# Optimization experiments

Hardware: AMD Instinct MI355X
Metric: run time of the kernel (lower is better)

The kernel has to match this reference:

```python
import jax, jax.numpy as jnp
import numpy as np

GROUPS = 8
NEG_SLOPE = 0.1
EPS = 1e-5


def group_norm(x, gamma, beta):
    # x: (B, N, C). Matches torch GroupNorm applied on (B, C, N):
    # normalize over (channels-in-group, N) per batch per group.
    B, N, C = x.shape
    xg = x.reshape(B, N, GROUPS, C // GROUPS)
    mean = xg.mean(axis=(1, 3), keepdims=True)
    var = xg.var(axis=(1, 3), keepdims=True)
    xg = (xg - mean) * jax.lax.rsqrt(var + EPS)
    return xg.reshape(B, N, C) * gamma + beta


def unary_block(x, W, b, gamma, beta):
    # Linear -> GroupNorm -> LeakyReLU(0.1)
    h = jnp.einsum('bnc,cd->bnd', x, W) + b
    h = group_norm(h, gamma, beta)
    return jnp.where(h >= 0, h, NEG_SLOPE * h)


def setup_inputs() -> dict:
    key = jax.random.key(0)
    ks = jax.random.split(key, 16)
    B, N, M, K, Cin, Cout = 4, 8192, 32768, 16, 128, 128
    inp = {
        'q_feats': jax.random.normal(ks[0], (B, N, Cin), jnp.float32),
        's_feats': jax.random.normal(ks[1], (B, M, Cin), jnp.float32),
        'q_points': jax.random.normal(ks[2], (B, N, 3), jnp.float32),
        's_points': jax.random.normal(ks[3], (B, N, K, 3), jnp.float32),
        'downsample_indices': jax.random.randint(ks[4], (B, N, K), 0, M, jnp.int32),
    }
    sc1 = 1.0 / np.sqrt(Cin)
    sc2 = 1.0 / np.sqrt(Cout)
    inp['W1'] = jax.random.uniform(ks[5], (Cin, Cout), jnp.float32, -sc1, sc1)
    inp['b1'] = jnp.zeros((Cout,), jnp.float32)
    inp['g1'] = jnp.ones((Cout,), jnp.float32)
    inp['be1'] = jnp.zeros((Cout,), jnp.float32)
    inp['W2'] = jax.random.uniform(ks[6], (Cout, Cout), jnp.float32, -sc2, sc2)
    inp['b2'] = jnp.zeros((Cout,), jnp.float32)
    inp['g2'] = jnp.ones((Cout,), jnp.float32)
    inp['be2'] = jnp.zeros((Cout,), jnp.float32)
    inp['W3'] = jax.random.uniform(ks[7], (Cout, Cout), jnp.float32, -sc2, sc2)
    inp['b3'] = jnp.zeros((Cout,), jnp.float32)
    inp['g3'] = jnp.ones((Cout,), jnp.float32)
    inp['be3'] = jnp.zeros((Cout,), jnp.float32)
    return inp


def reference(q_feats, s_feats, q_points, s_points, downsample_indices,
              W1, b1, g1, be1, W2, b2, g2, be2, W3, b3, g3, be3):
    # knn_gather: (B, N, K, C) gathered from (B, M, C)
    grouped = jax.vmap(lambda f, i: f[i])(s_feats, downsample_indices)
    # inverse-squared-distance weights over K neighbors
    d2 = jnp.sum((s_points - q_points[:, :, None, :]) ** 2, axis=-1)  # (B,N,K)
    w = 1.0 / (d2 + 1e-8)
    w = w / jnp.sum(w, axis=-1, keepdims=True)
    latent = jnp.sum(grouped * w[..., None], axis=2)  # (B,N,C)
    h = unary_block(latent, W1, b1, g1, be1)
    h = unary_block(h, W2, b2, g2, be2)
    return unary_block(h + q_feats, W3, b3, g3, be3)
```

## Files before the change

### kernel.cpp

```cpp
#include <hip/hip_runtime.h>


constexpr int NPB = 8192;
constexpr int BN  = 32768;
constexpr int CH  = 128;
constexpr int KNB = 16;
constexpr int MS  = 32768;
constexpr int NG  = 8;
constexpr int CG  = 16;
constexpr int RPB = 64;
constexpr int NBLK = BN / RPB;
constexpr int BPB  = NPB / RPB;
constexpr int XS = 152;
constexpr int WS = 152;

typedef short short8 __attribute__((ext_vector_type(8)));
typedef float floatx4 __attribute__((ext_vector_type(4)));

static __device__ __forceinline__ unsigned short f2bs(float f) {
    unsigned int u = __builtin_bit_cast(unsigned int, f);
    unsigned int r = (u + 0x7fffu + ((u >> 16) & 1u)) >> 16;
    return (unsigned short)r;
}
static __device__ __forceinline__ float bs2f(unsigned short s) {
    unsigned int u = ((unsigned int)s) << 16;
    return __builtin_bit_cast(float, u);
}

__global__ __launch_bounds__(256) void k_prep(
    const float* __restrict__ W1, const float* __restrict__ W2,
    const float* __restrict__ W3,
    unsigned short* __restrict__ Wt1, unsigned short* __restrict__ Wf2,
    unsigned short* __restrict__ Wf3)
{
    const int bi = blockIdx.x;
    const int w  = bi >> 6;
    const int i  = bi & 63;
    const int el = i * 256 + threadIdx.x;
    const int n  = el >> 7, k = el & 127;
    const float* W = (w == 0) ? W1 : (w == 1) ? W2 : W3;
    unsigned short v = f2bs(W[k * 128 + n]);
    if (w == 0) {
        Wt1[n * 128 + k] = v;
    } else {
        unsigned short* Wf = (w == 1) ? Wf2 : Wf3;
        int j = n >> 4, lr = n & 15;
        int kt = k >> 5, qd = (k >> 3) & 3, e = k & 7;
        Wf[(((j * 4 + kt) * 64) + (qd * 16 + lr)) * 8 + e] = v;
    }
}

__global__ __launch_bounds__(256) void k_head(
    const float* __restrict__ sf, const float* __restrict__ qp,
    const float* __restrict__ sp, const int* __restrict__ idx,
    const unsigned short* __restrict__ Wt,
    const float* __restrict__ bias,
    unsigned short* __restrict__ hout,
    float* __restrict__ part_out)
{
    const int bi = blockIdx.x;
    const int t  = threadIdx.x;
    const int b  = bi / BPB;

    __shared__ unsigned short Xl[RPB * XS];
    __shared__ unsigned short Wl[CH * WS];
    __shared__ float wv[RPB * KNB];
    __shared__ float winv[RPB];
    __shared__ float pw[4][16];

    #pragma unroll
    for (int i = 0; i < 8; i++) {
        int el = i * 2048 + t * 8;
        short8 w8 = *(const short8*)(Wt + el);
        *(short8*)&Wl[(el >> 7) * WS + (el & 127)] = w8;
    }

    #pragma unroll
    for (int i = 0; i < 4; i++) {
        int p = i * 256 + t;
        int row = p >> 4, k = p & 15;
        size_t rg = (size_t)bi * RPB + row;
        float qx = qp[rg * 3 + 0], qy = qp[rg * 3 + 1], qz = qp[rg * 3 + 2];
        const float* spp = sp + (rg * KNB + k) * 3;
        float dx = spp[0] - qx, dy = spp[1] - qy, dz = spp[2] - qz;
        wv[p] = 1.0f / (dx * dx + dy * dy + dz * dz + 1e-8f);
    }
    __syncthreads();
    if (t < RPB) {
        float s = 0.f;
        #pragma unroll
        for (int k = 0; k < KNB; k++) s += wv[t * KNB + k];
        winv[t] = 1.0f / s;
    }
    __syncthreads();
    {
        const int grp = t >> 5, c4 = (t & 31) * 4;
        for (int rr = 0; rr < 8; rr++) {
            int row = grp * 8 + rr;
            size_t rg = (size_t)bi * RPB + row;
            const int* ip = idx + rg * KNB;
            float ax = 0.f, ay = 0.f, az = 0.f, aw = 0.f;
            #pragma unroll
            for (int k = 0; k < KNB; k++) {
                int j = ip[k];
                const float4 f = *(const float4*)(sf + ((size_t)b * MS + j) * CH + c4);
                float w = wv[row * KNB + k];
                ax += w * f.x; ay += w * f.y; az += w * f.z; aw += w * f.w;
            }
            float wi = winv[row];
            ushort4 pk;
            pk.x = f2bs(ax * wi); pk.y = f2bs(ay * wi);
            pk.z = f2bs(az * wi); pk.w = f2bs(aw * wi);
            *(ushort4*)&Xl[row * XS + c4] = pk;
        }
    }
    __syncthreads();

    const int w  = t >> 6;
    const int l  = t & 63;
    const int lr = l & 15;
    const int qd = l >> 4;
    floatx4 acc[8] = {};
    #pragma unroll
    for (int kt = 0; kt < 4; kt++) {
        short8 a = *(const short8*)&Xl[(w * 16 + lr) * XS + kt * 32 + qd * 8];
        #pragma unroll
        for (int j = 0; j < 8; j++) {
            short8 bf = *(const short8*)&Wl[(j * 16 + lr) * WS + kt * 32 + qd * 8];
            acc[j] = __builtin_amdgcn_mfma_f32_16x16x32_bf16(a, bf, acc[j], 0, 0, 0);
        }
    }

    float vals[8][4];
    #pragma unroll
    for (int j = 0; j < 8; j++) {
        float bj = bias[j * 16 + lr];
        float ss = 0.f, qq = 0.f;
        #pragma unroll
        for (int r = 0; r < 4; r++) {
            float v = acc[j][r] + bj;
            vals[j][r] = v;
            ss += v; qq += v * v;
        }
        #pragma unroll
        for (int off = 32; off; off >>= 1) {
            ss += __shfl_down(ss, off);
            qq += __shfl_down(qq, off);
        }
        if (l == 0) { pw[w][j] = ss; pw[w][8 + j] = qq; }
    }
    #pragma unroll
    for (int j = 0; j < 8; j++)
        #pragma unroll
        for (int r = 0; r < 4; r++)
            Xl[(w * 16 + qd * 4 + r) * XS + j * 16 + lr] = f2bs(vals[j][r]);
    __syncthreads();
    if (t < 16)
        part_out[(size_t)bi * 16 + t] = pw[0][t] + pw[1][t] + pw[2][t] + pw[3][t];
    #pragma unroll
    for (int i = 0; i < 4; i++) {
        int flat = i * 2048 + t * 8;
        int row = flat >> 7, col = flat & 127;
        *(short8*)(hout + (size_t)bi * RPB * CH + flat) =
            *(const short8*)&Xl[row * XS + col];
    }
}

template <int RESID>
__global__ __launch_bounds__(256) void k_mid(
    const unsigned short* __restrict__ hin,
    const float* __restrict__ part_in,
    const float* __restrict__ gamma,
    const float* __restrict__ beta,
    const float* __restrict__ qf,
    const unsigned short* __restrict__ Wf,
    const float* __restrict__ bias,
    unsigned short* __restrict__ hout,
    float* __restrict__ part_out)
{
    const int bi = blockIdx.x;
    const int t  = threadIdx.x;
    const int b  = bi / BPB;

    __shared__ unsigned short Xl[RPB * XS];
    __shared__ float red[16][17];
    __shared__ float2 stats_s[NG];
    __shared__ float pw[4][16];

    {
        int j = t & 15, chunk = t >> 4;
        float acc = 0.f;
        #pragma unroll
        for (int i = 0; i < 8; i++)
            acc += part_in[(size_t)(b * BPB + chunk * 8 + i) * 16 + j];
        red[chunk][j] = acc;
    }
    __syncthreads();
    if (t < NG) {
        float s = 0.f, q = 0.f;
        #pragma unroll
        for (int c = 0; c < 16; c++) { s += red[c][t]; q += red[c][t + 8]; }
        const float cnt = (float)(NPB * CG);
        float mean = s / cnt;
        float var  = q / cnt - mean * mean;
        stats_s[t] = make_float2(mean, rsqrtf(var + 1e-5f));
    }
    __syncthreads();
    #pragma unroll
    for (int i = 0; i < 4; i++) {
        int flat = i * 2048 + t * 8;
        int row = flat >> 7, col = flat & 127;
        size_t gidx = (size_t)bi * RPB * CH + flat;
        short8 hv = *(const short8*)(hin + gidx);
        float2 st = stats_s[col >> 4];
        float4 g0 = *(const float4*)(gamma + col);
        float4 g1 = *(const float4*)(gamma + col + 4);
        float4 b0 = *(const float4*)(beta + col);
        float4 b1 = *(const float4*)(beta + col + 4);
        float gg[8] = {g0.x, g0.y, g0.z, g0.w, g1.x, g1.y, g1.z, g1.w};
        float bb[8] = {b0.x, b0.y, b0.z, b0.w, b1.x, b1.y, b1.z, b1.w};
        float re[8];
        if (RESID) {
            float4 r0 = *(const float4*)(qf + gidx);
            float4 r1 = *(const float4*)(qf + gidx + 4);
            re[0]=r0.x; re[1]=r0.y; re[2]=r0.z; re[3]=r0.w;
            re[4]=r1.x; re[5]=r1.y; re[6]=r1.z; re[7]=r1.w;
        }
        unsigned short ov[8];
        #pragma unroll
        for (int e = 0; e < 8; e++) {
            float v = bs2f((unsigned short)hv[e]);
            float y = (v - st.x) * st.y * gg[e] + bb[e];
            y = (y >= 0.f) ? y : 0.1f * y;
            if (RESID) y += re[e];
            ov[e] = f2bs(y);
        }
        *(short8*)&Xl[row * XS + col] = *(short8*)ov;
    }
    __syncthreads();

    const int w  = t >> 6;
    const int l  = t & 63;
    const int lr = l & 15;
    const int qd = l >> 4;
    floatx4 acc[8] = {};
    #pragma unroll
    for (int kt = 0; kt < 4; kt++) {
        short8 a = *(const short8*)&Xl[(w * 16 + lr) * XS + kt * 32 + qd * 8];
        #pragma unroll
        for (int j = 0; j < 8; j++) {
            short8 bf = *(const short8*)(Wf + (((j * 4 + kt) * 64) + l) * 8);
            acc[j] = __builtin_amdgcn_mfma_f32_16x16x32_bf16(a, bf, acc[j], 0, 0, 0);
        }
    }

    float vals[8][4];
    #pragma unroll
    for (int j = 0; j < 8; j++) {
        float bj = bias[j * 16 + lr];
        float ss = 0.f, qq = 0.f;
        #pragma unroll
        for (int r = 0; r < 4; r++) {
            float v = acc[j][r] + bj;
            vals[j][r] = v;
            ss += v; qq += v * v;
        }
        #pragma unroll
        for (int off = 32; off; off >>= 1) {
            ss += __shfl_down(ss, off);
            qq += __shfl_down(qq, off);
        }
        if (l == 0) { pw[w][j] = ss; pw[w][8 + j] = qq; }
    }
    #pragma unroll
    for (int j = 0; j < 8; j++)
        #pragma unroll
        for (int r = 0; r < 4; r++)
            Xl[(w * 16 + qd * 4 + r) * XS + j * 16 + lr] = f2bs(vals[j][r]);
    __syncthreads();
    if (t < 16)
        part_out[(size_t)bi * 16 + t] = pw[0][t] + pw[1][t] + pw[2][t] + pw[3][t];
    #pragma unroll
    for (int i = 0; i < 4; i++) {
        int flat = i * 2048 + t * 8;
        int row = flat >> 7, col = flat & 127;
        *(short8*)(hout + (size_t)bi * RPB * CH + flat) =
            *(const short8*)&Xl[row * XS + col];
    }
}

__global__ __launch_bounds__(256) void k_out(
    const unsigned short* __restrict__ hin, const float* __restrict__ part_in,
    const float* __restrict__ gamma, const float* __restrict__ beta,
    float* __restrict__ out)
{
    const int bi = blockIdx.x;
    const int t  = threadIdx.x;
    const int b  = bi / BPB;
    __shared__ float red[16][17];
    __shared__ float2 stats_s[NG];
    {
        int j = t & 15, chunk = t >> 4;
        float acc = 0.f;
        #pragma unroll
        for (int i = 0; i < 8; i++)
            acc += part_in[(size_t)(b * BPB + chunk * 8 + i) * 16 + j];
        red[chunk][j] = acc;
    }
    __syncthreads();
    if (t < NG) {
        float s = 0.f, q = 0.f;
        #pragma unroll
        for (int c = 0; c < 16; c++) { s += red[c][t]; q += red[c][t + 8]; }
        const float cnt = (float)(NPB * CG);
        float mean = s / cnt;
        float var  = q / cnt - mean * mean;
        stats_s[t] = make_float2(mean, rsqrtf(var + 1e-5f));
    }
    __syncthreads();
    #pragma unroll
    for (int i = 0; i < 4; i++) {
        int flat = i * 2048 + t * 8;
        int col = flat & 127;
        size_t gidx = (size_t)bi * RPB * CH + flat;
        short8 hv = *(const short8*)(hin + gidx);
        float2 st = stats_s[col >> 4];
        float4 g0 = *(const float4*)(gamma + col);
        float4 g1 = *(const float4*)(gamma + col + 4);
        float4 b0 = *(const float4*)(beta + col);
        float4 b1 = *(const float4*)(beta + col + 4);
        float gg[8] = {g0.x, g0.y, g0.z, g0.w, g1.x, g1.y, g1.z, g1.w};
        float bb[8] = {b0.x, b0.y, b0.z, b0.w, b1.x, b1.y, b1.z, b1.w};
        float o[8];
        #pragma unroll
        for (int e = 0; e < 8; e++) {
            float v = bs2f((unsigned short)hv[e]);
            float y = (v - st.x) * st.y * gg[e] + bb[e];
            o[e] = (y >= 0.f) ? y : 0.1f * y;
        }
        float4 o0 = {o[0], o[1], o[2], o[3]};
        float4 o1 = {o[4], o[5], o[6], o[7]};
        *(float4*)(out + gidx)     = o0;
        *(float4*)(out + gidx + 4) = o1;
    }
}

extern "C" void kernel_launch(void* const* d_in, const int* in_sizes, int n_in,
                              void* d_out, int out_size, void* d_ws, size_t ws_size,
                              hipStream_t stream) {
    const float* qf  = (const float*)d_in[0];
    const float* sf  = (const float*)d_in[1];
    const float* qp  = (const float*)d_in[2];
    const float* sp  = (const float*)d_in[3];
    const int*   idx = (const int*)  d_in[4];
    const float* W1  = (const float*)d_in[5];
    const float* b1  = (const float*)d_in[6];
    const float* g1  = (const float*)d_in[7];
    const float* be1 = (const float*)d_in[8];
    const float* W2  = (const float*)d_in[9];
    const float* b2  = (const float*)d_in[10];
    const float* g2  = (const float*)d_in[11];
    const float* be2 = (const float*)d_in[12];
    const float* W3  = (const float*)d_in[13];
    const float* b3  = (const float*)d_in[14];
    const float* g3  = (const float*)d_in[15];
    const float* be3 = (const float*)d_in[16];

    char* ws = (char*)d_ws;
    unsigned short* Wt1 = (unsigned short*)(ws);
    unsigned short* Wf2 = (unsigned short*)(ws + 32768);
    unsigned short* Wf3 = (unsigned short*)(ws + 65536);
    float* p1 = (float*)(ws + 98304);
    float* p2 = (float*)(ws + 131072);
    float* p3 = (float*)(ws + 163840);
    unsigned short* h1 = (unsigned short*)(ws + 196608);
    unsigned short* h2 = (unsigned short*)(ws + 196608 + 8388608);
    unsigned short* h3 = (unsigned short*)(ws + 196608 + 2 * 8388608);
    float* out = (float*)d_out;

    k_prep<<<192, 256, 0, stream>>>(W1, W2, W3, Wt1, Wf2, Wf3);
    k_head<<<NBLK, 256, 0, stream>>>(sf, qp, sp, idx, Wt1, b1, h1, p1);
    k_mid<0><<<NBLK, 256, 0, stream>>>(h1, p1, g1, be1, nullptr, Wf2, b2, h2, p2);
    k_mid<1><<<NBLK, 256, 0, stream>>>(h2, p2, g2, be2, qf, Wf3, b3, h3, p3);
    k_out<<<NBLK, 256, 0, stream>>>(h3, p3, g3, be3, out);
}
```

Measured before the change: 198.1 us.

## Shrink mid and output kernel tiles to 16 rows to raise block count

Result: no change. 195.2 us (-1.5%).

```diff
diff --git a/kernel.cpp b/kernel.cpp
--- a/kernel.cpp
+++ b/kernel.cpp
@@ -11,6 +11,9 @@
 constexpr int RPB = 64;
 constexpr int NBLK = BN / RPB;
 constexpr int BPB  = NPB / RPB;
+constexpr int MRPB = 16;
+constexpr int MNBLK = BN / MRPB;
+constexpr int MBPB  = NPB / MRPB;
 constexpr int XS = 152;
 constexpr int WS = 152;
 
@@ -166,7 +169,7 @@
     }
 }
 
-template <int RESID>
+template <int RESID, int PPB>
 __global__ __launch_bounds__(256) void k_mid(
     const unsigned short* __restrict__ hin,
     const float* __restrict__ part_in,
@@ -180,19 +183,20 @@
 {
     const int bi = blockIdx.x;
     const int t  = threadIdx.x;
-    const int b  = bi / BPB;
-
-    __shared__ unsigned short Xl[RPB * XS];
+    const int b  = bi / MBPB;
+
+    __shared__ unsigned short Xl[MRPB * XS];
     __shared__ float red[16][17];
     __shared__ float2 stats_s[NG];
-    __shared__ float pw[4][16];
-
+    __shared__ float pw[4][4];
+
+    constexpr int R = PPB / 16;
     {
         int j = t & 15, chunk = t >> 4;
         float acc = 0.f;
         #pragma unroll
-        for (int i = 0; i < 8; i++)
-            acc += part_in[(size_t)(b * BPB + chunk * 8 + i) * 16 + j];
+        for (int i = 0; i < R; i++)
+            acc += part_in[(size_t)(b * PPB + chunk * R + i) * 16 + j];
         red[chunk][j] = acc;
     }
     __syncthreads();
@@ -206,11 +210,11 @@
         stats_s[t] = make_float2(mean, rsqrtf(var + 1e-5f));
     }
     __syncthreads();
-    #pragma unroll
-    for (int i = 0; i < 4; i++) {
-        int flat = i * 2048 + t * 8;
+
+    {
+        int flat = t * 8;
         int row = flat >> 7, col = flat & 127;
-        size_t gidx = (size_t)bi * RPB * CH + flat;
+        size_t gidx = (size_t)bi * (MRPB * CH) + flat;
         short8 hv = *(const short8*)(hin + gidx);
         float2 st = stats_s[col >> 4];
         float4 g0 = *(const float4*)(gamma + col);
@@ -243,26 +247,28 @@
     const int l  = t & 63;
     const int lr = l & 15;
     const int qd = l >> 4;
-    floatx4 acc[8] = {};
+    floatx4 acc2[2] = {};
     #pragma unroll
     for (int kt = 0; kt < 4; kt++) {
-        short8 a = *(const short8*)&Xl[(w * 16 + lr) * XS + kt * 32 + qd * 8];
-        #pragma unroll
-        for (int j = 0; j < 8; j++) {
+        short8 a = *(const short8*)&Xl[lr * XS + kt * 32 + qd * 8];
+        #pragma unroll
+        for (int jj = 0; jj < 2; jj++) {
+            int j = w * 2 + jj;
             short8 bf = *(const short8*)(Wf + (((j * 4 + kt) * 64) + l) * 8);
-            acc[j] = __builtin_amdgcn_mfma_f32_16x16x32_bf16(a, bf, acc[j], 0, 0, 0);
-        }
-    }
-
-    float vals[8][4];
-    #pragma unroll
-    for (int j = 0; j < 8; j++) {
+            acc2[jj] = __builtin_amdgcn_mfma_f32_16x16x32_bf16(a, bf, acc2[jj], 0, 0, 0);
+        }
+    }
+
+    float vals[2][4];
+    #pragma unroll
+    for (int jj = 0; jj < 2; jj++) {
+        int j = w * 2 + jj;
         float bj = bias[j * 16 + lr];
         float ss = 0.f, qq = 0.f;
         #pragma unroll
         for (int r = 0; r < 4; r++) {
-            float v = acc[j][r] + bj;
-            vals[j][r] = v;
+            float v = acc2[jj][r] + bj;
+            vals[jj][r] = v;
             ss += v; qq += v * v;
         }
         #pragma unroll
@@ -270,21 +276,27 @@
             ss += __shfl_down(ss, off);
             qq += __shfl_down(qq, off);
         }
-        if (l == 0) { pw[w][j] = ss; pw[w][8 + j] = qq; }
-    }
-    #pragma unroll
-    for (int j = 0; j < 8; j++)
+        if (l == 0) { pw[w][jj] = ss; pw[w][2 + jj] = qq; }
+    }
+    __syncthreads();
+
+    #pragma unroll
+    for (int jj = 0; jj < 2; jj++)
         #pragma unroll
         for (int r = 0; r < 4; r++)
-            Xl[(w * 16 + qd * 4 + r) * XS + j * 16 + lr] = f2bs(vals[j][r]);
-    __syncthreads();
-    if (t < 16)
-        part_out[(size_t)bi * 16 + t] = pw[0][t] + pw[1][t] + pw[2][t] + pw[3][t];
-    #pragma unroll
-    for (int i = 0; i < 4; i++) {
-        int flat = i * 2048 + t * 8;
+            Xl[(qd * 4 + r) * XS + (w * 2 + jj) * 16 + lr] = f2bs(vals[jj][r]);
+    if (t < 8)
+        part_out[(size_t)bi * 16 + t] = pw[t >> 1][t & 1];
+    else if (t < 16) {
+        int g = t - 8;
+        part_out[(size_t)bi * 16 + t] = pw[g >> 1][2 + (g & 1)];
+    }
+    __syncthreads();
+
+    {
+        int flat = t * 8;
         int row = flat >> 7, col = flat & 127;
-        *(short8*)(hout + (size_t)bi * RPB * CH + flat) =
+        *(short8*)(hout + (size_t)bi * (MRPB * CH) + flat) =
             *(const short8*)&Xl[row * XS + col];
     }
 }
@@ -296,15 +308,17 @@
 {
     const int bi = blockIdx.x;
     const int t  = threadIdx.x;
-    const int b  = bi / BPB;
+    const int b  = bi / MBPB;
     __shared__ float red[16][17];
     __shared__ float2 stats_s[NG];
+    constexpr int PPB = 512;
+    constexpr int R = PPB / 16;
     {
         int j = t & 15, chunk = t >> 4;
         float acc = 0.f;
         #pragma unroll
-        for (int i = 0; i < 8; i++)
-            acc += part_in[(size_t)(b * BPB + chunk * 8 + i) * 16 + j];
+        for (int i = 0; i < R; i++)
+            acc += part_in[(size_t)(b * PPB + chunk * R + i) * 16 + j];
         red[chunk][j] = acc;
     }
     __syncthreads();
@@ -318,11 +332,10 @@
         stats_s[t] = make_float2(mean, rsqrtf(var + 1e-5f));
     }
     __syncthreads();
-    #pragma unroll
-    for (int i = 0; i < 4; i++) {
-        int flat = i * 2048 + t * 8;
+    {
+        int flat = t * 8;
         int col = flat & 127;
-        size_t gidx = (size_t)bi * RPB * CH + flat;
+        size_t gidx = (size_t)bi * (MRPB * CH) + flat;
         short8 hv = *(const short8*)(hin + gidx);
         float2 st = stats_s[col >> 4];
         float4 g0 = *(const float4*)(gamma + col);
@@ -372,15 +385,15 @@
     unsigned short* Wf3 = (unsigned short*)(ws + 65536);
     float* p1 = (float*)(ws + 98304);
     float* p2 = (float*)(ws + 131072);
-    float* p3 = (float*)(ws + 163840);
-    unsigned short* h1 = (unsigned short*)(ws + 196608);
-    unsigned short* h2 = (unsigned short*)(ws + 196608 + 8388608);
-    unsigned short* h3 = (unsigned short*)(ws + 196608 + 2 * 8388608);
+    float* p3 = (float*)(ws + 262144);
+    unsigned short* h1 = (unsigned short*)(ws + 393216);
+    unsigned short* h2 = (unsigned short*)(ws + 393216 + 8388608);
+    unsigned short* h3 = (unsigned short*)(ws + 393216 + 2 * 8388608);
     float* out = (float*)d_out;
 
     k_prep<<<192, 256, 0, stream>>>(W1, W2, W3, Wt1, Wf2, Wf3);
     k_head<<<NBLK, 256, 0, stream>>>(sf, qp, sp, idx, Wt1, b1, h1, p1);
-    k_mid<0><<<NBLK, 256, 0, stream>>>(h1, p1, g1, be1, nullptr, Wf2, b2, h2, p2);
-    k_mid<1><<<NBLK, 256, 0, stream>>>(h2, p2, g2, be2, qf, Wf3, b3, h3, p3);
-    k_out<<<NBLK, 256, 0, stream>>>(h3, p3, g3, be3, out);
-}
+    k_mid<0, 128><<<MNBLK, 256, 0, stream>>>(h1, p1, g1, be1, nullptr, Wf2, b2, h2, p2);
+    k_mid<1, 512><<<MNBLK, 256, 0, stream>>>(h2, p2, g2, be2, qf, Wf3, b3, h3, p3);
+    k_out<<<MNBLK, 256, 0, stream>>>(h3, p3, g3, be3, out);
+}
```
